# Kernel tuning notes

Measured on AMD Instinct MI355X. Metric: run time of the kernel, lower is better.

Reference implementation:

```python
import jax, jax.numpy as jnp
import numpy as np

UNITS = 20

def _lstm(x, W, U, b, return_sequences):
    # Keras LSTM with activation='relu', recurrent_activation='sigmoid'.
    # Gate order in kernels: i, f, c(g), o. x: [B,T,F], W: [F,4H], U: [H,4H], b: [4H]
    B = x.shape[0]
    H = U.shape[0]
    xW = jnp.einsum('btf,fg->btg', x, W) + b  # precompute input projection [B,T,4H]
    xW_t = jnp.swapaxes(xW, 0, 1)  # [T,B,4H]

    def step(carry, xw):
        h, c = carry
        z = xw + h @ U  # [B,4H]
        i = jax.nn.sigmoid(z[:, 0*H:1*H])
        f = jax.nn.sigmoid(z[:, 1*H:2*H])
        g = jax.nn.relu(z[:, 2*H:3*H])
        o = jax.nn.sigmoid(z[:, 3*H:4*H])
        c = f * c + i * g
        h = o * jax.nn.relu(c)
        return (h, c), h

    init = (jnp.zeros((B, H), x.dtype), jnp.zeros((B, H), x.dtype))
    (h_last, _), hs = jax.lax.scan(step, init, xW_t)
    if return_sequences:
        return jnp.swapaxes(hs, 0, 1)  # [B,T,H]
    return h_last  # [B,H]


def setup_inputs() -> dict:
    key = jax.random.key(0)
    ks = jax.random.split(key, 9)
    B, T, F, H = 2048, 256, 64, UNITS
    s_in = 1.0 / np.sqrt(F)
    s_h = 1.0 / np.sqrt(H)
    return {
        'x':  jax.random.normal(ks[0], (B, T, F), jnp.float32),
        'W1': jax.random.normal(ks[1], (F, 4 * H), jnp.float32) * s_in,
        'U1': jax.random.normal(ks[2], (H, 4 * H), jnp.float32) * s_h,
        'b1': jnp.zeros((4 * H,), jnp.float32),
        'W2': jax.random.normal(ks[3], (H, 4 * H), jnp.float32) * s_h,
        'U2': jax.random.normal(ks[4], (H, 4 * H), jnp.float32) * s_h,
        'b2': jnp.zeros((4 * H,), jnp.float32),
        'Wd': jax.random.normal(ks[5], (H, 1), jnp.float32) * s_h,
        'bd': jnp.zeros((1,), jnp.float32),
    }


def reference(x, W1, U1, b1, W2, U2, b2, Wd, bd):
    # Reshape is identity here (input already [B, T, F]).
    h1 = _lstm(x, W1, U1, b1, return_sequences=True)   # [B,T,20]
    h2 = _lstm(h1, W2, U2, b2, return_sequences=False)  # [B,20]
    return h2 @ Wd + bd  # [B,1]
```

## Files before the change

kernel.cpp:

```cpp
#include <hip/hip_runtime.h>
#include <math.h>

#define TT 256
#define FF 64
#define HH 20
#define G4 80
#define EPB 4
#define PBLK 320
#define RBLK 640
#define BLOB_BYTES 19456
#define WTHI_OFF 19456
#define WTLO_OFF 29696
#define XW_OFF   40960

typedef __attribute__((ext_vector_type(8))) short short8x;
typedef __attribute__((ext_vector_type(4))) float f32x4;

__device__ __forceinline__ float sigmoidf_(float z) {
    return __builtin_amdgcn_rcpf(1.0f + __expf(-z));
}
__device__ __forceinline__ float qpx1(float v) {
    return __int_as_float(__builtin_amdgcn_mov_dpp(__float_as_int(v), 0xB1, 0xF, 0xF, true));
}
__device__ __forceinline__ float qpx2(float v) {
    return __int_as_float(__builtin_amdgcn_mov_dpp(__float_as_int(v), 0x4E, 0xF, 0xF, true));
}
__device__ __forceinline__ float qpx3(float v) {
    return __int_as_float(__builtin_amdgcn_mov_dpp(__float_as_int(v), 0x1B, 0xF, 0xF, true));
}
__device__ __forceinline__ unsigned short bft(float f) {
    return (unsigned short)(__float_as_uint(f) >> 16);
}

__global__ void wprep(const float* __restrict__ U1, const float* __restrict__ W2,
                      const float* __restrict__ U2, const float* __restrict__ W1,
                      float4* __restrict__ blob,
                      unsigned short* __restrict__ wthi, unsigned short* __restrict__ wtlo) {
    int i = threadIdx.x + blockIdx.x * blockDim.x;
    if (i < 15 * G4) {
        int q = i / G4, j = i - q * G4;
        int m = q / 5, kq = q - m * 5;
        int col = (j & 3) * HH + (j >> 2);
        const float* M = (m == 0) ? U1 : (m == 1) ? W2 : U2;
        float4 v;
        v.x = M[(kq * 4 + 0) * G4 + col];
        v.y = M[(kq * 4 + 1) * G4 + col];
        v.z = M[(kq * 4 + 2) * G4 + col];
        v.w = M[(kq * 4 + 3) * G4 + col];
        blob[i] = v;
    } else if (i < 15 * G4 + FF * G4) {
        int idx = i - 15 * G4;
        int col = idx / FF, f = idx - col * FF;
        float w = W1[f * G4 + col];
        unsigned short h = bft(w);
        float fh = __uint_as_float((unsigned)h << 16);
        wthi[col * FF + f] = h;
        wtlo[col * FF + f] = bft(w - fh);
    }
}

__global__ __launch_bounds__(256, 4) void proj_mfma(
    const float* __restrict__ x,
    const unsigned short* __restrict__ wthi, const unsigned short* __restrict__ wtlo,
    const float* __restrict__ b1, float* __restrict__ xw, int B)
{
    __shared__ unsigned short Bthi[G4][72];
    __shared__ unsigned short Btlo[G4][72];
    const int tid = threadIdx.x;
    const int l   = tid & 63;
    const int w   = tid >> 6;
    const int b   = blockIdx.x >> 1;
    const int t0  = (blockIdx.x & 1) * 128;
    const int lane16 = l & 15;
    const int lgrp   = l >> 4;

    for (int c = tid; c < G4 * FF / 8; c += 256) {
        int row = c >> 3, cc = (c & 7) * 8;
        *(short8x*)&Bthi[row][cc] = *(const short8x*)&wthi[row * FF + cc];
        *(short8x*)&Btlo[row][cc] = *(const short8x*)&wtlo[row * FF + cc];
    }
    __syncthreads();

    float bias[5];
#pragma unroll
    for (int nt = 0; nt < 5; ++nt) bias[nt] = b1[nt * 16 + lane16];

    f32x4 acc[2][5];
#pragma unroll
    for (int mt = 0; mt < 2; ++mt)
#pragma unroll
        for (int nt = 0; nt < 5; ++nt) acc[mt][nt] = (f32x4){0.f, 0.f, 0.f, 0.f};

#pragma unroll
    for (int mt = 0; mt < 2; ++mt) {
        short8x Ah[2], Al[2];
        const int trow = t0 + w * 32 + mt * 16 + lane16;
        const float* xr = x + ((size_t)b * TT + trow) * FF + lgrp * 8;
#pragma unroll
        for (int ks = 0; ks < 2; ++ks) {
            float4 va = *(const float4*)(xr + ks * 32);
            float4 vb = *(const float4*)(xr + ks * 32 + 4);
            float v[8] = {va.x, va.y, va.z, va.w, vb.x, vb.y, vb.z, vb.w};
#pragma unroll
            for (int e = 0; e < 8; ++e) {
                unsigned short h = bft(v[e]);
                float fh = __uint_as_float((unsigned)h << 16);
                Ah[ks][e] = (short)h;
                Al[ks][e] = (short)bft(v[e] - fh);
            }
        }
#pragma unroll
        for (int nt = 0; nt < 5; ++nt) {
#pragma unroll
            for (int ks = 0; ks < 2; ++ks) {
                short8x bh = *(const short8x*)&Bthi[nt * 16 + lane16][ks * 32 + lgrp * 8];
                short8x bl = *(const short8x*)&Btlo[nt * 16 + lane16][ks * 32 + lgrp * 8];
                acc[mt][nt] = __builtin_amdgcn_mfma_f32_16x16x32_bf16(Ah[ks], bh, acc[mt][nt], 0, 0, 0);
                acc[mt][nt] = __builtin_amdgcn_mfma_f32_16x16x32_bf16(Al[ks], bh, acc[mt][nt], 0, 0, 0);
                acc[mt][nt] = __builtin_amdgcn_mfma_f32_16x16x32_bf16(Ah[ks], bl, acc[mt][nt], 0, 0, 0);
            }
        }
    }

#pragma unroll
    for (int mt = 0; mt < 2; ++mt) {
        const int trb = t0 + w * 32 + mt * 16 + lgrp * 4;
#pragma unroll
        for (int nt = 0; nt < 5; ++nt) {
            const int col = nt * 16 + lane16;
#pragma unroll
            for (int r = 0; r < 4; ++r) {
                xw[((size_t)(trb + r) * B + b) * G4 + col] = acc[mt][nt][r] + bias[nt];
            }
        }
    }
}

__global__ __launch_bounds__(RBLK, 2) void lstm2_pc(
    const float* __restrict__ xw, const float4* __restrict__ blob,
    const float* __restrict__ b2,
    const float* __restrict__ Wd, const float* __restrict__ bd,
    float* __restrict__ out, int B)
{
    const int tid  = threadIdx.x;
    const bool isL1 = tid < 320;
    const int rt   = isL1 ? tid : tid - 320;
    const int elem = rt / G4;
    const int j    = rt - elem * G4;
    const int g    = j & 3;
    const int u    = j >> 2;
    const int col  = g * HH + u;
    const int b0   = blockIdx.x * EPB;

    __shared__ float h1b[2][EPB][24];
    __shared__ float h2b[2][EPB][24];

    const float4* wb4 = blob + j;
    float wA[HH], wB[HH];
    if (isL1) {
#pragma unroll
        for (int q = 0; q < 5; ++q) {
            float4 v = wb4[q * G4];
            wA[4*q+0] = v.x; wA[4*q+1] = v.y; wA[4*q+2] = v.z; wA[4*q+3] = v.w;
        }
    } else {
#pragma unroll
        for (int q = 0; q < 5; ++q) {
            float4 v = wb4[(5 + q) * G4];
            wA[4*q+0] = v.x; wA[4*q+1] = v.y; wA[4*q+2] = v.z; wA[4*q+3] = v.w;
            float4 v2 = wb4[(10 + q) * G4];
            wB[4*q+0] = v2.x; wB[4*q+1] = v2.y; wB[4*q+2] = v2.z; wB[4*q+3] = v2.w;
        }
    }
    const float bias = isL1 ? 0.f : b2[col];

    for (int i = tid; i < 2 * EPB * 24; i += RBLK) ((float*)h1b)[i] = 0.f;
    for (int i = tid; i < 2 * EPB * 24; i += RBLK) ((float*)h2b)[i] = 0.f;

    const size_t tstride = (size_t)B * G4;
    const float* xwp = xw + (size_t)(b0 + elem) * G4 + col;
    float xwc = isL1 ? xwp[0] : 0.f;
    xwp += tstride;
    float c1 = 0.f, c2 = 0.f;
    __syncthreads();

    for (int i = 0; i <= TT; ++i) {
        const int rb = (i + 1) & 1;
        const int wb = i & 1;

        if (isL1 && i < TT) {
            float xwn = 0.f;
            if (i + 1 < TT) xwn = *xwp;
            xwp += tstride;

            float zz0 = 0.f, zz1 = 0.f, zz2 = 0.f, zz3 = 0.f;
            const float4* hv = (const float4*)h1b[rb][elem];
#pragma unroll
            for (int q = 0; q < HH / 4; ++q) {
                float4 hh = hv[q];
                zz0 = fmaf(hh.x, wA[4*q+0], zz0);
                zz1 = fmaf(hh.y, wA[4*q+1], zz1);
                zz2 = fmaf(hh.z, wA[4*q+2], zz2);
                zz3 = fmaf(hh.w, wA[4*q+3], zz3);
            }
            float z = xwc + ((zz0 + zz1) + (zz2 + zz3));

            float a = (g == 2) ? fmaxf(z, 0.f) : sigmoidf_(z);
            float a1 = qpx1(a), a2 = qpx2(a), a3 = qpx3(a);
            c1 = a1 * c1 + a * a2;
            float h1n = a3 * fmaxf(c1, 0.f);
            if (g == 0) h1b[wb][elem][u] = h1n;
            xwc = xwn;
        }
        if (!isL1 && i >= 1) {
            float y0 = 0.f, y1 = 0.f, y2 = 0.f, y3 = 0.f;
            const float4* h1v = (const float4*)h1b[rb][elem];
            const float4* h2v = (const float4*)h2b[rb][elem];
#pragma unroll
            for (int q = 0; q < HH / 4; ++q) {
                float4 ha = h1v[q];
                float4 hb = h2v[q];
                y0 = fmaf(ha.x, wA[4*q+0], y0);
                y1 = fmaf(ha.y, wA[4*q+1], y1);
                y2 = fmaf(ha.z, wA[4*q+2], y2);
                y3 = fmaf(ha.w, wA[4*q+3], y3);
                y0 = fmaf(hb.x, wB[4*q+0], y0);
                y1 = fmaf(hb.y, wB[4*q+1], y1);
                y2 = fmaf(hb.z, wB[4*q+2], y2);
                y3 = fmaf(hb.w, wB[4*q+3], y3);
            }
            float z2v = bias + ((y0 + y1) + (y2 + y3));

            float bgt = (g == 2) ? fmaxf(z2v, 0.f) : sigmoidf_(z2v);
            float b1_ = qpx1(bgt), b2_ = qpx2(bgt), b3_ = qpx3(bgt);
            c2 = b1_ * c2 + bgt * b2_;
            float h2n = b3_ * fmaxf(c2, 0.f);
            if (g == 0) h2b[wb][elem][u] = h2n;
        }
        __syncthreads();
    }

    if (tid < EPB) {
        float acc = bd[0];
#pragma unroll
        for (int k = 0; k < HH; ++k) acc += h2b[0][tid][k] * Wd[k];
        out[b0 + tid] = acc;
    }
}

__global__ __launch_bounds__(PBLK, 2) void lstm2_fused_fb(
    const float* __restrict__ x,
    const float* __restrict__ W1, const float* __restrict__ U1, const float* __restrict__ b1,
    const float* __restrict__ W2, const float* __restrict__ U2, const float* __restrict__ b2,
    const float* __restrict__ Wd, const float* __restrict__ bd,
    float* __restrict__ out)
{
    const int tid  = threadIdx.x;
    const int elem = tid / G4;
    const int j    = tid - elem * G4;
    const int g    = j & 3;
    const int u    = j >> 2;
    const int col  = g * HH + u;
    const int b0   = blockIdx.x * EPB;

    __shared__ float xs[2][EPB][FF];
    __shared__ float h1b[2][EPB][24];
    __shared__ float h2b[2][EPB][24];

    float w1[FF], u1[HH], w2[HH], u2[HH];
#pragma unroll
    for (int f = 0; f < FF; ++f) w1[f] = W1[f * G4 + col];
#pragma unroll
    for (int k = 0; k < HH; ++k) u1[k] = U1[k * G4 + col];
#pragma unroll
    for (int k = 0; k < HH; ++k) w2[k] = W2[k * G4 + col];
#pragma unroll
    for (int k = 0; k < HH; ++k) u2[k] = U2[k * G4 + col];
    const float bias1 = b1[col];
    const float bias2 = b2[col];

    for (int i = tid; i < 2 * EPB * 24; i += PBLK) ((float*)h1b)[i] = 0.f;
    for (int i = tid; i < 2 * EPB * 24; i += PBLK) ((float*)h2b)[i] = 0.f;
    if (tid < EPB * FF) {
        int e2 = tid >> 6, f2 = tid & 63;
        xs[0][e2][f2] = x[((long)(b0 + e2) * TT + 0) * FF + f2];
    }
    __syncthreads();

    float c1 = 0.f, c2 = 0.f;
    for (int t = 0; t < TT; ++t) {
        const int cur = t & 1;
        float xpre = 0.f;
        if (t + 1 < TT && tid < EPB * FF) {
            int e2 = tid >> 6, f2 = tid & 63;
            xpre = x[((long)(b0 + e2) * TT + (t + 1)) * FF + f2];
        }
        float zz0 = 0.f, zz1 = 0.f, zz2 = 0.f, zz3 = 0.f;
        const float4* xv = (const float4*)xs[cur][elem];
#pragma unroll
        for (int q = 0; q < FF / 4; ++q) {
            float4 xx = xv[q];
            zz0 = fmaf(xx.x, w1[4*q+0], zz0);
            zz1 = fmaf(xx.y, w1[4*q+1], zz1);
            zz2 = fmaf(xx.z, w1[4*q+2], zz2);
            zz3 = fmaf(xx.w, w1[4*q+3], zz3);
        }
        const float4* hv = (const float4*)h1b[cur][elem];
#pragma unroll
        for (int q = 0; q < HH / 4; ++q) {
            float4 hh = hv[q];
            zz0 = fmaf(hh.x, u1[4*q+0], zz0);
            zz1 = fmaf(hh.y, u1[4*q+1], zz1);
            zz2 = fmaf(hh.z, u1[4*q+2], zz2);
            zz3 = fmaf(hh.w, u1[4*q+3], zz3);
        }
        float z = bias1 + ((zz0 + zz1) + (zz2 + zz3));
        float a = (g == 2) ? fmaxf(z, 0.f) : sigmoidf_(z);
        float a1 = qpx1(a), a2 = qpx2(a), a3 = qpx3(a);
        c1 = a1 * c1 + a * a2;
        float h1n = a3 * fmaxf(c1, 0.f);
        if (g == 0) h1b[cur ^ 1][elem][u] = h1n;
        __syncthreads();
        if (t + 1 < TT && tid < EPB * FF) xs[cur ^ 1][tid >> 6][tid & 63] = xpre;

        float y0 = 0.f, y1 = 0.f, y2 = 0.f, y3 = 0.f;
        const float4* h1v = (const float4*)h1b[cur ^ 1][elem];
        const float4* h2v = (const float4*)h2b[cur][elem];
#pragma unroll
        for (int q = 0; q < HH / 4; ++q) {
            float4 ha = h1v[q];
            float4 hb = h2v[q];
            y0 = fmaf(ha.x, w2[4*q+0], y0);
            y1 = fmaf(ha.y, w2[4*q+1], y1);
            y2 = fmaf(ha.z, w2[4*q+2], y2);
            y3 = fmaf(ha.w, w2[4*q+3], y3);
            y0 = fmaf(hb.x, u2[4*q+0], y0);
            y1 = fmaf(hb.y, u2[4*q+1], y1);
            y2 = fmaf(hb.z, u2[4*q+2], y2);
            y3 = fmaf(hb.w, u2[4*q+3], y3);
        }
        float z2v = bias2 + ((y0 + y1) + (y2 + y3));
        float bgt = (g == 2) ? fmaxf(z2v, 0.f) : sigmoidf_(z2v);
        float b1_ = qpx1(bgt), b2_ = qpx2(bgt), b3_ = qpx3(bgt);
        c2 = b1_ * c2 + bgt * b2_;
        float h2n = b3_ * fmaxf(c2, 0.f);
        if (g == 0) h2b[cur ^ 1][elem][u] = h2n;
        __syncthreads();
    }
    if (j == 0) {
        float acc = bd[0];
#pragma unroll
        for (int k = 0; k < HH; ++k) acc += h2b[0][elem][k] * Wd[k];
        out[b0 + elem] = acc;
    }
}

extern "C" void kernel_launch(void* const* d_in, const int* in_sizes, int n_in,
                              void* d_out, int out_size, void* d_ws, size_t ws_size,
                              hipStream_t stream) {
    const float* x  = (const float*)d_in[0];
    const float* W1 = (const float*)d_in[1];
    const float* U1 = (const float*)d_in[2];
    const float* b1 = (const float*)d_in[3];
    const float* W2 = (const float*)d_in[4];
    const float* U2 = (const float*)d_in[5];
    const float* b2 = (const float*)d_in[6];
    const float* Wd = (const float*)d_in[7];
    const float* bd = (const float*)d_in[8];
    float* out = (float*)d_out;
    const int B = in_sizes[0] / (TT * FF);

    const size_t need = (size_t)XW_OFF + (size_t)B * TT * G4 * sizeof(float);
    if (ws_size >= need) {
        float4* blob = (float4*)d_ws;
        unsigned short* wthi = (unsigned short*)((char*)d_ws + WTHI_OFF);
        unsigned short* wtlo = (unsigned short*)((char*)d_ws + WTLO_OFF);
        float* xw = (float*)((char*)d_ws + XW_OFF);
        hipLaunchKernelGGL(wprep, dim3(26), dim3(256), 0, stream,
                           U1, W2, U2, W1, blob, wthi, wtlo);
        hipLaunchKernelGGL(proj_mfma, dim3(B * 2), dim3(256), 0, stream,
                           x, wthi, wtlo, b1, xw, B);
        hipLaunchKernelGGL(lstm2_pc, dim3(B / EPB), dim3(RBLK), 0, stream,
                           xw, blob, b2, Wd, bd, out, B);
    } else {
        hipLaunchKernelGGL(lstm2_fused_fb, dim3(B / EPB), dim3(PBLK), 0, stream,
                           x, W1, U1, b1, W2, U2, b2, Wd, bd, out);
    }
}
```

Measured before the change: 214.5 us.

## Fuse input projection into recurrent kernel with producer wavefront and LDS ring

Removes the separate MFMA projection kernel and its large global xW buffer. A third role (one extra wavefront per block) computes the input projection with split-bf16 MFMA in bursts of 4 timesteps into an 8-slot shared-memory ring, which the layer-1 threads read in place of global loads. W1 columns are permuted so the ring uses the per-thread gate order. This avoids writing and re-reading about 168 MB of projection data, at the cost of a larger block, more shared memory per block, and projection work on the recurrent critical path between barriers.

```diff
diff --git a/kernel.cpp b/kernel.cpp
--- a/kernel.cpp
+++ b/kernel.cpp
@@ -5,13 +5,12 @@
 #define FF 64
 #define HH 20
 #define G4 80
-#define EPB 4
 #define PBLK 320
-#define RBLK 640
+#define RBLK 704
 #define BLOB_BYTES 19456
 #define WTHI_OFF 19456
 #define WTLO_OFF 29696
-#define XW_OFF   40960
+#define WS_NEED  39936
 
 typedef __attribute__((ext_vector_type(8))) short short8x;
 typedef __attribute__((ext_vector_type(4))) float f32x4;
@@ -50,52 +49,86 @@
         blob[i] = v;
     } else if (i < 15 * G4 + FF * G4) {
         int idx = i - 15 * G4;
-        int col = idx / FF, f = idx - col * FF;
+        int p = idx / FF, f = idx - p * FF;
+        int col = (p & 3) * HH + (p >> 2);
         float w = W1[f * G4 + col];
         unsigned short h = bft(w);
         float fh = __uint_as_float((unsigned)h << 16);
-        wthi[col * FF + f] = h;
-        wtlo[col * FF + f] = bft(w - fh);
-    }
-}
-
-__global__ __launch_bounds__(256, 4) void proj_mfma(
-    const float* __restrict__ x,
+        wthi[p * FF + f] = h;
+        wtlo[p * FF + f] = bft(w - fh);
+    }
+}
+
+__global__ __launch_bounds__(RBLK, 6) void lstm2_all(
+    const float* __restrict__ x, const float4* __restrict__ blob,
     const unsigned short* __restrict__ wthi, const unsigned short* __restrict__ wtlo,
-    const float* __restrict__ b1, float* __restrict__ xw, int B)
+    const float* __restrict__ b1, const float* __restrict__ b2,
+    const float* __restrict__ Wd, const float* __restrict__ bd,
+    float* __restrict__ out, int B)
 {
+    const int tid = threadIdx.x;
+    const int b0  = blockIdx.x * 4;
+
+    __shared__ float h1b[2][4][24];
+    __shared__ float h2b[2][4][24];
+    __shared__ float ring[8][4][84];
     __shared__ unsigned short Bthi[G4][72];
     __shared__ unsigned short Btlo[G4][72];
-    const int tid = threadIdx.x;
-    const int l   = tid & 63;
-    const int w   = tid >> 6;
-    const int b   = blockIdx.x >> 1;
-    const int t0  = (blockIdx.x & 1) * 128;
-    const int lane16 = l & 15;
-    const int lgrp   = l >> 4;
-
-    for (int c = tid; c < G4 * FF / 8; c += 256) {
+
+    for (int c = tid; c < G4 * FF / 8; c += RBLK) {
         int row = c >> 3, cc = (c & 7) * 8;
         *(short8x*)&Bthi[row][cc] = *(const short8x*)&wthi[row * FF + cc];
         *(short8x*)&Btlo[row][cc] = *(const short8x*)&wtlo[row * FF + cc];
     }
-    __syncthreads();
-
-    float bias[5];
-#pragma unroll
-    for (int nt = 0; nt < 5; ++nt) bias[nt] = b1[nt * 16 + lane16];
-
-    f32x4 acc[2][5];
-#pragma unroll
-    for (int mt = 0; mt < 2; ++mt)
-#pragma unroll
-        for (int nt = 0; nt < 5; ++nt) acc[mt][nt] = (f32x4){0.f, 0.f, 0.f, 0.f};
-
-#pragma unroll
-    for (int mt = 0; mt < 2; ++mt) {
+    for (int i = tid; i < 2 * 4 * 24; i += RBLK) ((float*)h1b)[i] = 0.f;
+    for (int i = tid; i < 2 * 4 * 24; i += RBLK) ((float*)h2b)[i] = 0.f;
+
+    const int role = (tid < 320) ? 0 : (tid < 640) ? 1 : 2;
+
+    const int rt   = (role == 1) ? tid - 320 : tid;
+    const int elem = (rt / G4) & 3;
+    const int j    = rt - (rt / G4) * G4;
+    const int g    = j & 3;
+    const int u    = j >> 2;
+    const int col  = g * HH + u;
+
+    float wA[HH], wB[HH];
+    float bias = 0.f;
+    if (role == 0) {
+        const float4* wb4 = blob + j;
+#pragma unroll
+        for (int q = 0; q < 5; ++q) {
+            float4 v = wb4[q * G4];
+            wA[4*q+0] = v.x; wA[4*q+1] = v.y; wA[4*q+2] = v.z; wA[4*q+3] = v.w;
+        }
+    } else if (role == 1) {
+        const float4* wb4 = blob + j;
+#pragma unroll
+        for (int q = 0; q < 5; ++q) {
+            float4 v = wb4[(5 + q) * G4];
+            wA[4*q+0] = v.x; wA[4*q+1] = v.y; wA[4*q+2] = v.z; wA[4*q+3] = v.w;
+            float4 v2 = wb4[(10 + q) * G4];
+            wB[4*q+0] = v2.x; wB[4*q+1] = v2.y; wB[4*q+2] = v2.z; wB[4*q+3] = v2.w;
+        }
+        bias = b2[col];
+    }
+
+    const int pl  = tid - 640;
+    const int i0  = pl & 15;
+    const int lg  = pl >> 4;
+    const int ae  = i0 >> 2, at = i0 & 3;
+    float biasp[5];
+    if (role == 2) {
+#pragma unroll
+        for (int nt = 0; nt < 5; ++nt) {
+            int p = nt * 16 + i0;
+            biasp[nt] = b1[(p & 3) * HH + (p >> 2)];
+        }
+    }
+
+    auto burst = [&](int tb) {
         short8x Ah[2], Al[2];
-        const int trow = t0 + w * 32 + mt * 16 + lane16;
-        const float* xr = x + ((size_t)b * TT + trow) * FF + lgrp * 8;
+        const float* xr = x + ((size_t)(b0 + ae) * TT + (tb + at)) * FF + lg * 8;
 #pragma unroll
         for (int ks = 0; ks < 2; ++ks) {
             float4 va = *(const float4*)(xr + ks * 32);
@@ -111,76 +144,26 @@
         }
 #pragma unroll
         for (int nt = 0; nt < 5; ++nt) {
+            f32x4 acc = (f32x4){0.f, 0.f, 0.f, 0.f};
 #pragma unroll
             for (int ks = 0; ks < 2; ++ks) {
-                short8x bh = *(const short8x*)&Bthi[nt * 16 + lane16][ks * 32 + lgrp * 8];
-                short8x bl = *(const short8x*)&Btlo[nt * 16 + lane16][ks * 32 + lgrp * 8];
-                acc[mt][nt] = __builtin_amdgcn_mfma_f32_16x16x32_bf16(Ah[ks], bh, acc[mt][nt], 0, 0, 0);
-                acc[mt][nt] = __builtin_amdgcn_mfma_f32_16x16x32_bf16(Al[ks], bh, acc[mt][nt], 0, 0, 0);
-                acc[mt][nt] = __builtin_amdgcn_mfma_f32_16x16x32_bf16(Ah[ks], bl, acc[mt][nt], 0, 0, 0);
-            }
-        }
-    }
-
-#pragma unroll
-    for (int mt = 0; mt < 2; ++mt) {
-        const int trb = t0 + w * 32 + mt * 16 + lgrp * 4;
-#pragma unroll
-        for (int nt = 0; nt < 5; ++nt) {
-            const int col = nt * 16 + lane16;
+                short8x bh = *(const short8x*)&Bthi[nt * 16 + i0][ks * 32 + lg * 8];
+                short8x bl = *(const short8x*)&Btlo[nt * 16 + i0][ks * 32 + lg * 8];
+                acc = __builtin_amdgcn_mfma_f32_16x16x32_bf16(Ah[ks], bh, acc, 0, 0, 0);
+                acc = __builtin_amdgcn_mfma_f32_16x16x32_bf16(Al[ks], bh, acc, 0, 0, 0);
+                acc = __builtin_amdgcn_mfma_f32_16x16x32_bf16(Ah[ks], bl, acc, 0, 0, 0);
+            }
 #pragma unroll
             for (int r = 0; r < 4; ++r) {
-                xw[((size_t)(trb + r) * B + b) * G4 + col] = acc[mt][nt][r] + bias[nt];
-            }
-        }
-    }
-}
-
-__global__ __launch_bounds__(RBLK, 2) void lstm2_pc(
-    const float* __restrict__ xw, const float4* __restrict__ blob,
-    const float* __restrict__ b2,
-    const float* __restrict__ Wd, const float* __restrict__ bd,
-    float* __restrict__ out, int B)
-{
-    const int tid  = threadIdx.x;
-    const bool isL1 = tid < 320;
-    const int rt   = isL1 ? tid : tid - 320;
-    const int elem = rt / G4;
-    const int j    = rt - elem * G4;
-    const int g    = j & 3;
-    const int u    = j >> 2;
-    const int col  = g * HH + u;
-    const int b0   = blockIdx.x * EPB;
-
-    __shared__ float h1b[2][EPB][24];
-    __shared__ float h2b[2][EPB][24];
-
-    const float4* wb4 = blob + j;
-    float wA[HH], wB[HH];
-    if (isL1) {
-#pragma unroll
-        for (int q = 0; q < 5; ++q) {
-            float4 v = wb4[q * G4];
-            wA[4*q+0] = v.x; wA[4*q+1] = v.y; wA[4*q+2] = v.z; wA[4*q+3] = v.w;
-        }
-    } else {
-#pragma unroll
-        for (int q = 0; q < 5; ++q) {
-            float4 v = wb4[(5 + q) * G4];
-            wA[4*q+0] = v.x; wA[4*q+1] = v.y; wA[4*q+2] = v.z; wA[4*q+3] = v.w;
-            float4 v2 = wb4[(10 + q) * G4];
-            wB[4*q+0] = v2.x; wB[4*q+1] = v2.y; wB[4*q+2] = v2.z; wB[4*q+3] = v2.w;
-        }
-    }
-    const float bias = isL1 ? 0.f : b2[col];
-
-    for (int i = tid; i < 2 * EPB * 24; i += RBLK) ((float*)h1b)[i] = 0.f;
-    for (int i = tid; i < 2 * EPB * 24; i += RBLK) ((float*)h2b)[i] = 0.f;
-
-    const size_t tstride = (size_t)B * G4;
-    const float* xwp = xw + (size_t)(b0 + elem) * G4 + col;
-    float xwc = isL1 ? xwp[0] : 0.f;
-    xwp += tstride;
+                int row = lg * 4 + r;
+                ring[(tb + (row & 3)) & 7][row >> 2][nt * 16 + i0] = acc[r] + biasp[nt];
+            }
+        }
+    };
+
+    __syncthreads();
+
+    if (role == 2) { burst(0); burst(4); }
     float c1 = 0.f, c2 = 0.f;
     __syncthreads();
 
@@ -188,59 +171,58 @@
         const int rb = (i + 1) & 1;
         const int wb = i & 1;
 
-        if (isL1 && i < TT) {
-            float xwn = 0.f;
-            if (i + 1 < TT) xwn = *xwp;
-            xwp += tstride;
-
-            float zz0 = 0.f, zz1 = 0.f, zz2 = 0.f, zz3 = 0.f;
-            const float4* hv = (const float4*)h1b[rb][elem];
-#pragma unroll
-            for (int q = 0; q < HH / 4; ++q) {
-                float4 hh = hv[q];
-                zz0 = fmaf(hh.x, wA[4*q+0], zz0);
-                zz1 = fmaf(hh.y, wA[4*q+1], zz1);
-                zz2 = fmaf(hh.z, wA[4*q+2], zz2);
-                zz3 = fmaf(hh.w, wA[4*q+3], zz3);
-            }
-            float z = xwc + ((zz0 + zz1) + (zz2 + zz3));
-
-            float a = (g == 2) ? fmaxf(z, 0.f) : sigmoidf_(z);
-            float a1 = qpx1(a), a2 = qpx2(a), a3 = qpx3(a);
-            c1 = a1 * c1 + a * a2;
-            float h1n = a3 * fmaxf(c1, 0.f);
-            if (g == 0) h1b[wb][elem][u] = h1n;
-            xwc = xwn;
-        }
-        if (!isL1 && i >= 1) {
-            float y0 = 0.f, y1 = 0.f, y2 = 0.f, y3 = 0.f;
-            const float4* h1v = (const float4*)h1b[rb][elem];
-            const float4* h2v = (const float4*)h2b[rb][elem];
-#pragma unroll
-            for (int q = 0; q < HH / 4; ++q) {
-                float4 ha = h1v[q];
-                float4 hb = h2v[q];
-                y0 = fmaf(ha.x, wA[4*q+0], y0);
-                y1 = fmaf(ha.y, wA[4*q+1], y1);
-                y2 = fmaf(ha.z, wA[4*q+2], y2);
-                y3 = fmaf(ha.w, wA[4*q+3], y3);
-                y0 = fmaf(hb.x, wB[4*q+0], y0);
-                y1 = fmaf(hb.y, wB[4*q+1], y1);
-                y2 = fmaf(hb.z, wB[4*q+2], y2);
-                y3 = fmaf(hb.w, wB[4*q+3], y3);
-            }
-            float z2v = bias + ((y0 + y1) + (y2 + y3));
-
-            float bgt = (g == 2) ? fmaxf(z2v, 0.f) : sigmoidf_(z2v);
-            float b1_ = qpx1(bgt), b2_ = qpx2(bgt), b3_ = qpx3(bgt);
-            c2 = b1_ * c2 + bgt * b2_;
-            float h2n = b3_ * fmaxf(c2, 0.f);
-            if (g == 0) h2b[wb][elem][u] = h2n;
+        if (role == 0) {
+            if (i < TT) {
+                float xwc = ring[i & 7][elem][j];
+                float zz0 = 0.f, zz1 = 0.f, zz2 = 0.f, zz3 = 0.f;
+                const float4* hv = (const float4*)h1b[rb][elem];
+#pragma unroll
+                for (int q = 0; q < 5; ++q) {
+                    float4 hh = hv[q];
+                    zz0 = fmaf(hh.x, wA[4*q+0], zz0);
+                    zz1 = fmaf(hh.y, wA[4*q+1], zz1);
+                    zz2 = fmaf(hh.z, wA[4*q+2], zz2);
+                    zz3 = fmaf(hh.w, wA[4*q+3], zz3);
+                }
+                float z = xwc + ((zz0 + zz1) + (zz2 + zz3));
+                float a = (g == 2) ? fmaxf(z, 0.f) : sigmoidf_(z);
+                float a1 = qpx1(a), a2 = qpx2(a), a3 = qpx3(a);
+                c1 = a1 * c1 + a * a2;
+                float h1n = a3 * fmaxf(c1, 0.f);
+                if (g == 0) h1b[wb][elem][u] = h1n;
+            }
+        } else if (role == 1) {
+            if (i >= 1) {
+                float y0 = 0.f, y1 = 0.f, y2 = 0.f, y3 = 0.f;
+                const float4* h1v = (const float4*)h1b[rb][elem];
+                const float4* h2v = (const float4*)h2b[rb][elem];
+#pragma unroll
+                for (int q = 0; q < 5; ++q) {
+                    float4 ha = h1v[q];
+                    float4 hb = h2v[q];
+                    y0 = fmaf(ha.x, wA[4*q+0], y0);
+                    y1 = fmaf(ha.y, wA[4*q+1], y1);
+                    y2 = fmaf(ha.z, wA[4*q+2], y2);
+                    y3 = fmaf(ha.w, wA[4*q+3], y3);
+                    y0 = fmaf(hb.x, wB[4*q+0], y0);
+                    y1 = fmaf(hb.y, wB[4*q+1], y1);
+                    y2 = fmaf(hb.z, wB[4*q+2], y2);
+                    y3 = fmaf(hb.w, wB[4*q+3], y3);
+                }
+                float z2v = bias + ((y0 + y1) + (y2 + y3));
+                float bgt = (g == 2) ? fmaxf(z2v, 0.f) : sigmoidf_(z2v);
+                float b1_ = qpx1(bgt), b2_ = qpx2(bgt), b3_ = qpx3(bgt);
+                c2 = b1_ * c2 + bgt * b2_;
+                float h2n = b3_ * fmaxf(c2, 0.f);
+                if (g == 0) h2b[wb][elem][u] = h2n;
+            }
+        } else {
+            if ((i & 3) == 0 && i >= 4 && i <= TT - 8) burst(i + 4);
         }
         __syncthreads();
     }
 
-    if (tid < EPB) {
+    if (tid < 4) {
         float acc = bd[0];
 #pragma unroll
         for (int k = 0; k < HH; ++k) acc += h2b[0][tid][k] * Wd[k];
@@ -261,11 +243,11 @@
     const int g    = j & 3;
     const int u    = j >> 2;
     const int col  = g * HH + u;
-    const int b0   = blockIdx.x * EPB;
-
-    __shared__ float xs[2][EPB][FF];
-    __shared__ float h1b[2][EPB][24];
-    __shared__ float h2b[2][EPB][24];
+    const int b0   = blockIdx.x * 4;
+
+    __shared__ float xs[2][4][FF];
+    __shared__ float h1b[2][4][24];
+    __shared__ float h2b[2][4][24];
 
     float w1[FF], u1[HH], w2[HH], u2[HH];
 #pragma unroll
@@ -279,9 +261,9 @@
     const float bias1 = b1[col];
     const float bias2 = b2[col];
 
-    for (int i = tid; i < 2 * EPB * 24; i += PBLK) ((float*)h1b)[i] = 0.f;
-    for (int i = tid; i < 2 * EPB * 24; i += PBLK) ((float*)h2b)[i] = 0.f;
-    if (tid < EPB * FF) {
+    for (int i = tid; i < 2 * 4 * 24; i += PBLK) ((float*)h1b)[i] = 0.f;
+    for (int i = tid; i < 2 * 4 * 24; i += PBLK) ((float*)h2b)[i] = 0.f;
+    if (tid < 4 * FF) {
         int e2 = tid >> 6, f2 = tid & 63;
         xs[0][e2][f2] = x[((long)(b0 + e2) * TT + 0) * FF + f2];
     }
@@ -291,7 +273,7 @@
     for (int t = 0; t < TT; ++t) {
         const int cur = t & 1;
         float xpre = 0.f;
-        if (t + 1 < TT && tid < EPB * FF) {
+        if (t + 1 < TT && tid < 4 * FF) {
             int e2 = tid >> 6, f2 = tid & 63;
             xpre = x[((long)(b0 + e2) * TT + (t + 1)) * FF + f2];
         }
@@ -321,7 +303,7 @@
         float h1n = a3 * fmaxf(c1, 0.f);
         if (g == 0) h1b[cur ^ 1][elem][u] = h1n;
         __syncthreads();
-        if (t + 1 < TT && tid < EPB * FF) xs[cur ^ 1][tid >> 6][tid & 63] = xpre;
+        if (t + 1 < TT && tid < 4 * FF) xs[cur ^ 1][tid >> 6][tid & 63] = xpre;
 
         float y0 = 0.f, y1 = 0.f, y2 = 0.f, y3 = 0.f;
         const float4* h1v = (const float4*)h1b[cur ^ 1][elem];
@@ -370,20 +352,16 @@
     float* out = (float*)d_out;
     const int B = in_sizes[0] / (TT * FF);
 
-    const size_t need = (size_t)XW_OFF + (size_t)B * TT * G4 * sizeof(float);
-    if (ws_size >= need) {
+    if (ws_size >= (size_t)WS_NEED) {
         float4* blob = (float4*)d_ws;
         unsigned short* wthi = (unsigned short*)((char*)d_ws + WTHI_OFF);
         unsigned short* wtlo = (unsigned short*)((char*)d_ws + WTLO_OFF);
-        float* xw = (float*)((char*)d_ws + XW_OFF);
-        hipLaunchKernelGGL(wprep, dim3(26), dim3(256), 0, stream,
+        hipLaunchKernelGGL(wprep, dim3(25), dim3(256), 0, stream,
                            U1, W2, U2, W1, blob, wthi, wtlo);
-        hipLaunchKernelGGL(proj_mfma, dim3(B * 2), dim3(256), 0, stream,
-                           x, wthi, wtlo, b1, xw, B);
-        hipLaunchKernelGGL(lstm2_pc, dim3(B / EPB), dim3(RBLK), 0, stream,
-                           xw, blob, b2, Wd, bd, out, B);
+        hipLaunchKernelGGL(lstm2_all, dim3(B / 4), dim3(RBLK), 0, stream,
+                           x, blob, wthi, wtlo, b1, b2, Wd, bd, out, B);
     } else {
-        hipLaunchKernelGGL(lstm2_fused_fb, dim3(B / EPB), dim3(PBLK), 0, stream,
+        hipLaunchKernelGGL(lstm2_fused_fb, dim3(B / 4), dim3(PBLK), 0, stream,
                            x, W1, U1, b1, W2, U2, b2, Wd, bd, out);
     }
 }
```

Measured after the change: 608.6 us. +183.7%, slower.
